# Performance work log

Measured on AMD Instinct MI355X. Metric: run time of the kernel, lower is better.

## Reference

```python
import jax, jax.numpy as jnp
import numpy as np

HEADS = 2
BN_EPS = 1e-5


def _axial_self_attn(x, Wq, Wkv, Wout, bout):
    # x: (b, s, t, c) -- attend along t (the axial sequence dim)
    b, s, t, c = x.shape
    dh = c // HEADS
    q = (x @ Wq).reshape(b, s, t, HEADS, dh)
    k, v = jnp.split(x @ Wkv, 2, axis=-1)  # matches torch .chunk(2, dim=-1)
    k = k.reshape(b, s, t, HEADS, dh)
    v = v.reshape(b, s, t, HEADS, dh)
    dots = jnp.einsum('bsind,bsjnd->bsnij', q, k) * (dh ** -0.5)
    attn = jax.nn.softmax(dots, axis=-1)
    out = jnp.einsum('bsnij,bsjnd->bsind', attn, v).reshape(b, s, t, c)
    return out @ Wout + bout


def setup_inputs() -> dict:
    key = jax.random.key(0)
    ks = jax.random.split(key, 8)
    B, C, H, W = 8, 128, 256, 256
    E = 2 * C
    sd = 0.05
    return {
        'x': jax.random.normal(ks[0], (B, C, H, W), jnp.float32),
        'Wq_h': jax.random.normal(ks[1], (C, C), jnp.float32) * sd,
        'Wkv_h': jax.random.normal(ks[2], (C, 2 * C), jnp.float32) * sd,
        'Wout_h': jax.random.normal(ks[3], (C, C), jnp.float32) * sd,
        'bout_h': jnp.zeros((C,), jnp.float32),
        'Wq_w': jax.random.normal(ks[4], (C, C), jnp.float32) * sd,
        'Wkv_w': jax.random.normal(ks[5], (C, 2 * C), jnp.float32) * sd,
        'Wout_w': jax.random.normal(ks[6], (C, C), jnp.float32) * sd,
        'bout_w': jnp.zeros((C,), jnp.float32),
        'conv_w': jax.random.normal(ks[7], (E, E), jnp.float32) * sd,  # (in, out); torch conv weight[o,i,0,0].T
        'gamma': jnp.ones((E,), jnp.float32),
        'beta': jnp.zeros((E,), jnp.float32),
    }


def reference(x, Wq_h, Wkv_h, Wout_h, bout_h, Wq_w, Wkv_w, Wout_w, bout_w, conv_w, gamma, beta):
    B, C, H, W = x.shape
    # MaxPool2d(2)
    xp = x.reshape(B, C, H // 2, 2, W // 2, 2).max(axis=(3, 5))  # (B,C,H2,W2)
    xc = jnp.transpose(xp, (0, 2, 3, 1))  # (B,H2,W2,C) channels-last
    # AxialAttention, sum_axial_out=True: height-axis attn + width-axis attn
    a_h = _axial_self_attn(jnp.transpose(xc, (0, 2, 1, 3)), Wq_h, Wkv_h, Wout_h, bout_h)
    a_h = jnp.transpose(a_h, (0, 2, 1, 3))
    a_w = _axial_self_attn(xc, Wq_w, Wkv_w, Wout_w, bout_w)
    a = jax.nn.relu(a_h + a_w)
    # cat((x_attn, x), dim=channel) then conv1x1 -> relu -> BatchNorm (batch stats)
    y = jnp.concatenate([a, xc], axis=-1) @ conv_w  # (B,H2,W2,2C)
    y = jax.nn.relu(y)
    mean = y.mean(axis=(0, 1, 2))
    var = y.var(axis=(0, 1, 2))
    y = (y - mean) * jax.lax.rsqrt(var + BN_EPS) * gamma + beta
    return jnp.transpose(y, (0, 3, 1, 2))  # back to NCHW
```

## Files before the change

### kernel.cpp

```cpp
#include <hip/hip_runtime.h>
#include <hip/hip_bf16.h>


typedef short v8s __attribute__((ext_vector_type(8)));
typedef short v4s __attribute__((ext_vector_type(4)));
typedef float v4f __attribute__((ext_vector_type(4)));
typedef float v4flt __attribute__((ext_vector_type(4)));

#define LSA 136
#define LSC 264
#define LSY 72
#define LSP 130

static __device__ __forceinline__ short f2bf(float f){
  __hip_bfloat16 h = __float2bfloat16(f);
  return __builtin_bit_cast(short, h);
}
static __device__ __forceinline__ float bf2f(short s){
  unsigned u = ((unsigned)(unsigned short)s) << 16;
  return __builtin_bit_cast(float, u);
}

__global__ void prep_kernel(const float* __restrict__ Wq_h, const float* __restrict__ Wkv_h,
                            const float* __restrict__ Wout_h, const float* __restrict__ Wq_w,
                            const float* __restrict__ Wkv_w, const float* __restrict__ Wout_w,
                            const float* __restrict__ conv_w, short* __restrict__ wt,
                            float* __restrict__ stats){
  int idx = blockIdx.x * 256 + threadIdx.x;
  if (idx < 8192) stats[idx] = 0.0f;
  const float* src; int K, O, base;
  if      (idx <  16384){ base = 0;      K=128; O=128; src=Wq_h;  }
  else if (idx <  49152){ base = 16384;  K=128; O=256; src=Wkv_h; }
  else if (idx <  65536){ base = 49152;  K=128; O=128; src=Wout_h;}
  else if (idx <  81920){ base = 65536;  K=128; O=128; src=Wq_w;  }
  else if (idx < 114688){ base = 81920;  K=128; O=256; src=Wkv_w; }
  else if (idx < 131072){ base = 114688; K=128; O=128; src=Wout_w;}
  else                  { base = 131072; K=256; O=256; src=conv_w;}
  int local = idx - base;
  int o = local / K, i = local - o * K;
  wt[idx] = f2bf(src[i * O + o]);
}

__global__ __launch_bounds__(256, 4)
void pool_kernel(const float* __restrict__ x, short* __restrict__ xp){
  __shared__ short t_[128*LSP];
  int bx = blockIdx.x;
  int b = bx >> 7, i = bx & 127;
  int tid = (int)threadIdx.x;
  int j2 = tid & 63;
  int cq = tid >> 6;
  for (int rep = 0; rep < 32; ++rep){
    int c = cq*32 + rep;
    const float* p0 = x + (((b*128 + c)*256 + 2*i)*256 + 4*j2);
    v4flt a  = *(const v4flt*)p0;
    v4flt bb = *(const v4flt*)(p0 + 256);
    t_[(2*j2)*LSP + c]   = f2bf(fmaxf(fmaxf(a[0], a[1]), fmaxf(bb[0], bb[1])));
    t_[(2*j2+1)*LSP + c] = f2bf(fmaxf(fmaxf(a[2], a[3]), fmaxf(bb[2], bb[3])));
  }
  __syncthreads();
  int obase = ((b*128 + i)*128)*128;
  for (int rep = 0; rep < 8; ++rep){
    int idx = rep*256 + tid;
    int row = idx >> 4, seg = idx & 15;
    *(v8s*)(xp + obase + row*128 + seg*8) = *(const v8s*)(&t_[row*LSP + seg*8]);
  }
}

__global__ __launch_bounds__(512, 6)
void attn_kernel(const short* __restrict__ xp, const short* __restrict__ wt,
                 const float* __restrict__ bout_h, const float* __restrict__ bout_w,
                 short* __restrict__ ah, short* __restrict__ aw){
  __shared__ short A[128*LSA];
  __shared__ short WB[64*LSA];

  const int bx = blockIdx.x;
  const int dir = bx & 1;
  const int sb = bx >> 1;
  const int b = sb >> 7, s = sb & 127;
  const int tid = (int)threadIdx.x;
  const int w = tid >> 6;
  const int lane = tid & 63;
  const int l15 = lane & 15, l4 = lane >> 4;

  const short* Wq   = wt + dir*65536;
  const short* Wk   = Wq + 16384;
  const short* Wv   = Wq + 32768;
  const short* Wout = Wq + 49152;
  const float* bsrc = dir ? bout_w : bout_h;
  short*       ao   = dir ? aw : ah;

  const int trow = 16*w + l15;
  const int xbase = dir ? (((b*128 + s)*128 + trow)*128)
                        : (((b*128 + trow)*128 + s)*128);
  v8s av[4];
  #pragma unroll
  for (int kk = 0; kk < 4; ++kk)
    av[kk] = *(const v8s*)(xp + xbase + kk*32 + l4*8);

  v8s rw0, rw1;
#define LOAD_H(SRC, HF)                                                  \
  { rw0 = *(const v8s*)((SRC) + (64*(HF) + (tid>>4))*128 + (tid&15)*8);  \
    rw1 = *(const v8s*)((SRC) + (64*(HF) + 32 + (tid>>4))*128 + (tid&15)*8); }
#define WRITE_H()                                                        \
  { *(v8s*)(&WB[(tid>>4)*LSA + (tid&15)*8]) = rw0;                       \
    *(v8s*)(&WB[(32 + (tid>>4))*LSA + (tid&15)*8]) = rw1; }

#define QK_HALF(HF)                                                      \
  { _Pragma("unroll")                                                    \
    for (int tcl = 0; tcl < 4; ++tcl){                                   \
      int tc = 4*(HF) + tcl;                                             \
      v4f d = {0.f,0.f,0.f,0.f};                                         \
      _Pragma("unroll")                                                  \
      for (int kk = 0; kk < 4; ++kk){                                    \
        v8s bf = *(const v8s*)(&WB[(tcl*16 + l15)*LSA + kk*32 + l4*8]);  \
        d = __builtin_amdgcn_mfma_f32_16x16x32_bf16(av[kk], bf, d, 0, 0, 0); \
      }                                                                  \
      _Pragma("unroll")                                                  \
      for (int r = 0; r < 4; ++r)                                        \
        A[(16*w + 4*l4 + r)*LSA + 16*tc + l15] = f2bf(d[r]);             \
    } }

#define V_HALF(HF)                                                       \
  { _Pragma("unroll")                                                    \
    for (int tcl = 0; tcl < 4; ++tcl){                                   \
      int tc = 4*(HF) + tcl;                                             \
      v4f d = {0.f,0.f,0.f,0.f};                                         \
      _Pragma("unroll")                                                  \
      for (int kk = 0; kk < 4; ++kk){                                    \
        v8s bf = *(const v8s*)(&WB[(tcl*16 + l15)*LSA + kk*32 + l4*8]);  \
        d = __builtin_amdgcn_mfma_f32_16x16x32_bf16(av[kk], bf, d, 0, 0, 0); \
      }                                                                  \
      v4s pkv;                                                           \
      _Pragma("unroll")                                                  \
      for (int r = 0; r < 4; ++r) pkv[r] = f2bf(d[r]);                   \
      *(v4s*)(&A[(16*tc + l15)*LSA + 16*w + 4*l4]) = pkv;                \
    } }

#define OUTPROJ_HALF(HF)                                                 \
  { _Pragma("unroll")                                                    \
    for (int tcl = 0; tcl < 4; ++tcl){                                   \
      int tc = 4*(HF) + tcl;                                             \
      v4f d = {0.f,0.f,0.f,0.f};                                         \
      _Pragma("unroll")                                                  \
      for (int kk = 0; kk < 4; ++kk){                                    \
        v8s awf = *(const v8s*)(&WB[(tcl*16 + l15)*LSA + kk*32 + l4*8]); \
        d = __builtin_amdgcn_mfma_f32_16x16x32_bf16(awf, ob[kk], d, 0, 0, 0); \
      }                                                                  \
      v4f bias = *(const v4f*)(bsrc + 16*tc + 4*l4);                     \
      v4s z;                                                             \
      _Pragma("unroll")                                                  \
      for (int r = 0; r < 4; ++r) z[r] = f2bf(d[r] + bias[r]);           \
      *(v4s*)(&A[(16*w + l15)*LSA + 16*tc + 4*l4]) = z;                  \
    } }

  LOAD_H(Wq, 0);
  WRITE_H(); __syncthreads();
  LOAD_H(Wq, 1);
  QK_HALF(0); __syncthreads();
  WRITE_H(); __syncthreads();
  LOAD_H(Wk, 0);
  QK_HALF(1);
  v8s bq[2][2];
  #pragma unroll
  for (int h = 0; h < 2; ++h)
    #pragma unroll
    for (int kk = 0; kk < 2; ++kk)
      bq[h][kk] = *(const v8s*)(&A[(16*w + l15)*LSA + h*64 + kk*32 + l4*8]);
  __syncthreads();

  WRITE_H(); __syncthreads();
  LOAD_H(Wk, 1);
  QK_HALF(0); __syncthreads();
  WRITE_H(); __syncthreads();
  LOAD_H(Wv, 0);
  QK_HALF(1); __syncthreads();
  WRITE_H();

  v4s pk[2][8];
  #pragma unroll
  for (int h = 0; h < 2; ++h){
    v4f st[8];
    #pragma unroll
    for (int jt = 0; jt < 8; ++jt){
      v4f d = {0.f,0.f,0.f,0.f};
      #pragma unroll
      for (int kk = 0; kk < 2; ++kk){
        v8s ak = *(const v8s*)(&A[(16*jt + l15)*LSA + h*64 + kk*32 + l4*8]);
        d = __builtin_amdgcn_mfma_f32_16x16x32_bf16(ak, bq[h][kk], d, 0, 0, 0);
      }
      st[jt] = d;
    }
    float mx = -1e30f;
    #pragma unroll
    for (int jt = 0; jt < 8; ++jt)
      #pragma unroll
      for (int r = 0; r < 4; ++r) mx = fmaxf(mx, st[jt][r]);
    mx = fmaxf(mx, __shfl_xor(mx, 16));
    mx = fmaxf(mx, __shfl_xor(mx, 32));
    float sm = 0.f;
    #pragma unroll
    for (int jt = 0; jt < 8; ++jt)
      #pragma unroll
      for (int r = 0; r < 4; ++r){
        float e = __expf((st[jt][r] - mx) * 0.125f);
        st[jt][r] = e; sm += e;
      }
    sm += __shfl_xor(sm, 16);
    sm += __shfl_xor(sm, 32);
    float inv = 1.0f / sm;
    #pragma unroll
    for (int jt = 0; jt < 8; ++jt)
      #pragma unroll
      for (int r = 0; r < 4; ++r) pk[h][jt][r] = f2bf(st[jt][r] * inv);
  }
  __syncthreads();

  v8s pa[2][4];
  #pragma unroll
  for (int h = 0; h < 2; ++h){
    #pragma unroll
    for (int jt = 0; jt < 8; ++jt)
      *(v4s*)(&A[(16*w + l15)*LSA + 16*jt + 4*l4]) = pk[h][jt];
    #pragma unroll
    for (int kk = 0; kk < 4; ++kk)
      pa[h][kk] = *(const v8s*)(&A[(16*w + l15)*LSA + kk*32 + l4*8]);
  }
  __syncthreads();

  LOAD_H(Wv, 1);
  V_HALF(0); __syncthreads();
  WRITE_H(); __syncthreads();
  LOAD_H(Wout, 0);
  V_HALF(1); __syncthreads();
  WRITE_H();

  v4f ot[2][4];
  #pragma unroll
  for (int h = 0; h < 2; ++h)
    #pragma unroll
    for (int tc = 0; tc < 4; ++tc){
      v4f d = {0.f,0.f,0.f,0.f};
      #pragma unroll
      for (int kk = 0; kk < 4; ++kk){
        v8s vf = *(const v8s*)(&A[(64*h + 16*tc + l15)*LSA + kk*32 + l4*8]);
        d = __builtin_amdgcn_mfma_f32_16x16x32_bf16(vf, pa[h][kk], d, 0, 0, 0);
      }
      ot[h][tc] = d;
    }
  __syncthreads();

  #pragma unroll
  for (int h = 0; h < 2; ++h)
    #pragma unroll
    for (int tc = 0; tc < 4; ++tc){
      v4s pko;
      #pragma unroll
      for (int r = 0; r < 4; ++r) pko[r] = f2bf(ot[h][tc][r]);
      *(v4s*)(&A[(16*w + l15)*LSA + 64*h + 16*tc + 4*l4]) = pko;
    }
  v8s ob[4];
  #pragma unroll
  for (int kk = 0; kk < 4; ++kk)
    ob[kk] = *(const v8s*)(&A[(16*w + l15)*LSA + kk*32 + l4*8]);
  LOAD_H(Wout, 1);
  OUTPROJ_HALF(0);
  __syncthreads();
  WRITE_H(); __syncthreads();
  OUTPROJ_HALF(1);
  __syncthreads();

  int obase = ((b*128 + s)*128)*128;
  #pragma unroll
  for (int r = 0; r < 4; ++r){
    int idx = (r*512 + tid) * 8;
    int t = idx >> 7, c = idx & 127;
    *(v8s*)(ao + obase + t*128 + c) = *(const v8s*)(&A[t*LSA + c]);
  }
#undef LOAD_H
#undef WRITE_H
#undef QK_HALF
#undef V_HALF
#undef OUTPROJ_HALF
}

__global__ __launch_bounds__(512, 4)
void conv_kernel(const short* __restrict__ ah, const short* __restrict__ aw,
                 const short* __restrict__ xp, const short* __restrict__ wt,
                 short* __restrict__ yb, float* __restrict__ stats){
  __shared__ short cats[256*LSY];
  __shared__ float lsum[256];
  __shared__ float lsq[256];
  const short* convT = wt + 131072;
  int bx = blockIdx.x;
  int half = bx & 1;
  int row = bx >> 1;
  int b = row >> 7, ii = row & 127;
  int tid = (int)threadIdx.x;
  int wv = tid >> 6, lane = tid & 63, l15 = lane & 15, l4 = lane >> 4;
  if (tid < 256){ lsum[tid] = 0.f; lsq[tid] = 0.f; }

  v8s wf[2][8];
  #pragma unroll
  for (int x = 0; x < 2; ++x)
    #pragma unroll
    for (int kk = 0; kk < 8; ++kk)
      wf[x][kk] = *(const v8s*)(convT + (((wv + 8*x)*16 + l15)*256) + kk*32 + l4*8);

  #pragma unroll
  for (int r = 0; r < 2; ++r){
    int idx = (r*512 + tid) * 8;
    int t = idx >> 7, c = idx & 127;
    int tg = 64*half + t;
    v8s hv = *(const v8s*)(ah + ((b*128 + tg)*128 + ii)*128 + c);
    v8s wv_ = *(const v8s*)(aw + ((b*128 + ii)*128 + tg)*128 + c);
    v8s o;
    #pragma unroll
    for (int k = 0; k < 8; ++k)
      o[k] = f2bf(fmaxf(bf2f(hv[k]) + bf2f(wv_[k]), 0.f));
    *(v8s*)(&cats[t*LSC + c]) = o;
    *(v8s*)(&cats[t*LSC + 128 + c]) =
        *(const v8s*)(xp + ((b*128 + ii)*128 + tg)*128 + c);
  }
  __syncthreads();

  v4s ypk[2][4];
  float s1[2] = {0.f,0.f}, s2[2] = {0.f,0.f};
  #pragma unroll
  for (int tt = 0; tt < 4; ++tt){
    v4f d0 = {0.f,0.f,0.f,0.f}, d1 = {0.f,0.f,0.f,0.f};
    #pragma unroll
    for (int kk = 0; kk < 8; ++kk){
      v8s af = *(const v8s*)(&cats[(16*tt + l15)*LSC + kk*32 + l4*8]);
      d0 = __builtin_amdgcn_mfma_f32_16x16x32_bf16(af, wf[0][kk], d0, 0, 0, 0);
      d1 = __builtin_amdgcn_mfma_f32_16x16x32_bf16(af, wf[1][kk], d1, 0, 0, 0);
    }
    #pragma unroll
    for (int r = 0; r < 4; ++r){
      float y0 = fmaxf(d0[r], 0.f), y1 = fmaxf(d1[r], 0.f);
      ypk[0][tt][r] = f2bf(y0); ypk[1][tt][r] = f2bf(y1);
      s1[0] += y0; s2[0] += y0*y0;
      s1[1] += y1; s2[1] += y1*y1;
    }
  }
  #pragma unroll
  for (int x = 0; x < 2; ++x){
    s1[x] += __shfl_xor(s1[x], 16); s1[x] += __shfl_xor(s1[x], 32);
    s2[x] += __shfl_xor(s2[x], 16); s2[x] += __shfl_xor(s2[x], 32);
  }
  if (l4 == 0){
    #pragma unroll
    for (int x = 0; x < 2; ++x){
      int e = (wv + 8*x)*16 + l15;
      atomicAdd(&lsum[e], s1[x]);
      atomicAdd(&lsq[e],  s2[x]);
    }
  }
  __syncthreads();
  #pragma unroll
  for (int x = 0; x < 2; ++x)
    #pragma unroll
    for (int tt = 0; tt < 4; ++tt)
      *(v4s*)(&cats[((wv + 8*x)*16 + l15)*LSY + 16*tt + 4*l4]) = ypk[x][tt];
  __syncthreads();
  #pragma unroll
  for (int r = 0; r < 4; ++r){
    int idxv = r*512 + tid;
    int e = idxv >> 3, jseg = idxv & 7;
    *(v8s*)(yb + ((b*256 + e)*128 + ii)*128 + 64*half + jseg*8) =
        *(const v8s*)(&cats[e*LSY + jseg*8]);
  }
  if (tid < 256){
    int c = bx & 15;
    atomicAdd(&stats[c*512 + tid],       lsum[tid]);
    atomicAdd(&stats[c*512 + 256 + tid], lsq[tid]);
  }
}

__global__ void bn_kernel(const short* __restrict__ yb, float* __restrict__ out,
                          const float* __restrict__ stats,
                          const float* __restrict__ gamma, const float* __restrict__ beta){
  const float invn = 1.0f / 131072.0f;
  int bx = blockIdx.x;
  int e = bx & 255;
  float s1 = 0.f, s2 = 0.f;
  #pragma unroll
  for (int c = 0; c < 16; ++c){
    s1 += stats[c*512 + e];
    s2 += stats[c*512 + 256 + e];
  }
  float m   = s1 * invn;
  float var = s2 * invn - m * m;
  float sc  = gamma[e] * rsqrtf(var + 1e-5f);
  float sh  = beta[e] - m * sc;
  int base = bx * 16384;
  int tid = (int)threadIdx.x;
  for (int rep = 0; rep < 8; ++rep){
    int idx = base + (rep*256 + tid)*8;
    v8s yv = *(const v8s*)(yb + idx);
    v4f o1, o2;
    #pragma unroll
    for (int r = 0; r < 4; ++r){
      o1[r] = bf2f(yv[r])   * sc + sh;
      o2[r] = bf2f(yv[4+r]) * sc + sh;
    }
    *(v4f*)(out + idx)     = o1;
    *(v4f*)(out + idx + 4) = o2;
  }
}

extern "C" void kernel_launch(void* const* d_in, const int* in_sizes, int n_in,
                              void* d_out, int out_size, void* d_ws, size_t ws_size,
                              hipStream_t stream){
  const float* x      = (const float*)d_in[0];
  const float* Wq_h   = (const float*)d_in[1];
  const float* Wkv_h  = (const float*)d_in[2];
  const float* Wout_h = (const float*)d_in[3];
  const float* bout_h = (const float*)d_in[4];
  const float* Wq_w   = (const float*)d_in[5];
  const float* Wkv_w  = (const float*)d_in[6];
  const float* Wout_w = (const float*)d_in[7];
  const float* bout_w = (const float*)d_in[8];
  const float* conv_w = (const float*)d_in[9];
  const float* gamma  = (const float*)d_in[10];
  const float* beta   = (const float*)d_in[11];
  float* out = (float*)d_out;

  char* ws = (char*)d_ws;
  short* xp    = (short*)(ws);
  short* ah    = (short*)(ws +  33554432);
  short* aw    = (short*)(ws +  67108864);
  short* yb    = (short*)(ws + 100663296);
  short* wt    = (short*)(ws + 167772160);
  float* stats = (float*)(ws + 168165376);

  prep_kernel<<<768, 256, 0, stream>>>(Wq_h, Wkv_h, Wout_h, Wq_w, Wkv_w, Wout_w,
                                       conv_w, wt, stats);
  pool_kernel<<<1024, 256, 0, stream>>>(x, xp);
  attn_kernel<<<2048, 512, 0, stream>>>(xp, wt, bout_h, bout_w, ah, aw);
  conv_kernel<<<2048, 512, 0, stream>>>(ah, aw, xp, wt, yb, stats);
  bn_kernel<<<2048, 256, 0, stream>>>(yb, out, stats, gamma, beta);
}
```

Baseline: 257.7 us.

## Double-buffer weight quarters in attention and split pooling across channel halves

The attention kernel now stages weights in 32-row quarters through two LDS buffers. The next quarter's global load and LDS write are interleaved with MFMA work on the current buffer, so fewer syncthreads stall on weight staging. The pooling kernel is split into two blocks per row, each covering half the channels, with a smaller LDS tile and higher occupancy bounds. The attention schedule adds more barriers per phase and is intricate, so a mistake in buffer reuse ordering could cause races.

```diff
diff --git a/kernel.cpp b/kernel.cpp
--- a/kernel.cpp
+++ b/kernel.cpp
@@ -10,7 +10,7 @@
 #define LSA 136
 #define LSC 264
 #define LSY 72
-#define LSP 130
+#define LSQ 66
 
 static __device__ __forceinline__ short f2bf(float f){
   __hip_bfloat16 h = __float2bfloat16(f);
@@ -41,28 +41,32 @@
   wt[idx] = f2bf(src[i * O + o]);
 }
 
-__global__ __launch_bounds__(256, 4)
+__global__ __launch_bounds__(256, 8)
 void pool_kernel(const float* __restrict__ x, short* __restrict__ xp){
-  __shared__ short t_[128*LSP];
+  __shared__ short t_[128*LSQ];
   int bx = blockIdx.x;
-  int b = bx >> 7, i = bx & 127;
+  int chalf = bx & 1;
+  int row = bx >> 1;
+  int b = row >> 7, i = row & 127;
   int tid = (int)threadIdx.x;
   int j2 = tid & 63;
   int cq = tid >> 6;
-  for (int rep = 0; rep < 32; ++rep){
-    int c = cq*32 + rep;
+  for (int rep = 0; rep < 16; ++rep){
+    int cl = cq*16 + rep;
+    int c = chalf*64 + cl;
     const float* p0 = x + (((b*128 + c)*256 + 2*i)*256 + 4*j2);
     v4flt a  = *(const v4flt*)p0;
     v4flt bb = *(const v4flt*)(p0 + 256);
-    t_[(2*j2)*LSP + c]   = f2bf(fmaxf(fmaxf(a[0], a[1]), fmaxf(bb[0], bb[1])));
-    t_[(2*j2+1)*LSP + c] = f2bf(fmaxf(fmaxf(a[2], a[3]), fmaxf(bb[2], bb[3])));
-  }
-  __syncthreads();
-  int obase = ((b*128 + i)*128)*128;
-  for (int rep = 0; rep < 8; ++rep){
+    t_[(2*j2)*LSQ + cl]   = f2bf(fmaxf(fmaxf(a[0], a[1]), fmaxf(bb[0], bb[1])));
+    t_[(2*j2+1)*LSQ + cl] = f2bf(fmaxf(fmaxf(a[2], a[3]), fmaxf(bb[2], bb[3])));
+  }
+  __syncthreads();
+  int obase = ((b*128 + i)*128)*128 + chalf*64;
+  #pragma unroll
+  for (int rep = 0; rep < 4; ++rep){
     int idx = rep*256 + tid;
-    int row = idx >> 4, seg = idx & 15;
-    *(v8s*)(xp + obase + row*128 + seg*8) = *(const v8s*)(&t_[row*LSP + seg*8]);
+    int r_ = idx >> 3, seg = idx & 7;
+    *(v8s*)(xp + obase + r_*128 + seg*8) = *(const v8s*)(&t_[r_*LSQ + seg*8]);
   }
 }
 
@@ -71,7 +75,7 @@
                  const float* __restrict__ bout_h, const float* __restrict__ bout_w,
                  short* __restrict__ ah, short* __restrict__ aw){
   __shared__ short A[128*LSA];
-  __shared__ short WB[64*LSA];
+  __shared__ short WB[2][32*LSA];
 
   const int bx = blockIdx.x;
   const int dir = bx & 1;
@@ -81,6 +85,8 @@
   const int w = tid >> 6;
   const int lane = tid & 63;
   const int l15 = lane & 15, l4 = lane >> 4;
+  const int qrow = tid >> 4;
+  const int qseg = tid & 15;
 
   const short* Wq   = wt + dir*65536;
   const short* Wk   = Wq + 16384;
@@ -97,22 +103,18 @@
   for (int kk = 0; kk < 4; ++kk)
     av[kk] = *(const v8s*)(xp + xbase + kk*32 + l4*8);
 
-  v8s rw0, rw1;
-#define LOAD_H(SRC, HF)                                                  \
-  { rw0 = *(const v8s*)((SRC) + (64*(HF) + (tid>>4))*128 + (tid&15)*8);  \
-    rw1 = *(const v8s*)((SRC) + (64*(HF) + 32 + (tid>>4))*128 + (tid&15)*8); }
-#define WRITE_H()                                                        \
-  { *(v8s*)(&WB[(tid>>4)*LSA + (tid&15)*8]) = rw0;                       \
-    *(v8s*)(&WB[(32 + (tid>>4))*LSA + (tid&15)*8]) = rw1; }
-
-#define QK_HALF(HF)                                                      \
+  v8s rw;
+#define LOAD_Q(SRC, QI)  rw = *(const v8s*)((SRC) + (32*(QI) + qrow)*128 + qseg*8);
+#define WRITE_Q(SL)      *(v8s*)(&WB[SL][qrow*LSA + qseg*8]) = rw;
+
+#define QK_Q(SL, TB)                                                     \
   { _Pragma("unroll")                                                    \
-    for (int tcl = 0; tcl < 4; ++tcl){                                   \
-      int tc = 4*(HF) + tcl;                                             \
+    for (int tcl = 0; tcl < 2; ++tcl){                                   \
+      int tc = (TB) + tcl;                                               \
       v4f d = {0.f,0.f,0.f,0.f};                                         \
       _Pragma("unroll")                                                  \
       for (int kk = 0; kk < 4; ++kk){                                    \
-        v8s bf = *(const v8s*)(&WB[(tcl*16 + l15)*LSA + kk*32 + l4*8]);  \
+        v8s bf = *(const v8s*)(&WB[SL][(tcl*16 + l15)*LSA + kk*32 + l4*8]); \
         d = __builtin_amdgcn_mfma_f32_16x16x32_bf16(av[kk], bf, d, 0, 0, 0); \
       }                                                                  \
       _Pragma("unroll")                                                  \
@@ -120,14 +122,14 @@
         A[(16*w + 4*l4 + r)*LSA + 16*tc + l15] = f2bf(d[r]);             \
     } }
 
-#define V_HALF(HF)                                                       \
+#define V_Q(SL, TB)                                                      \
   { _Pragma("unroll")                                                    \
-    for (int tcl = 0; tcl < 4; ++tcl){                                   \
-      int tc = 4*(HF) + tcl;                                             \
+    for (int tcl = 0; tcl < 2; ++tcl){                                   \
+      int tc = (TB) + tcl;                                               \
       v4f d = {0.f,0.f,0.f,0.f};                                         \
       _Pragma("unroll")                                                  \
       for (int kk = 0; kk < 4; ++kk){                                    \
-        v8s bf = *(const v8s*)(&WB[(tcl*16 + l15)*LSA + kk*32 + l4*8]);  \
+        v8s bf = *(const v8s*)(&WB[SL][(tcl*16 + l15)*LSA + kk*32 + l4*8]); \
         d = __builtin_amdgcn_mfma_f32_16x16x32_bf16(av[kk], bf, d, 0, 0, 0); \
       }                                                                  \
       v4s pkv;                                                           \
@@ -136,14 +138,14 @@
       *(v4s*)(&A[(16*tc + l15)*LSA + 16*w + 4*l4]) = pkv;                \
     } }
 
-#define OUTPROJ_HALF(HF)                                                 \
+#define OP_Q(SL, TB)                                                     \
   { _Pragma("unroll")                                                    \
-    for (int tcl = 0; tcl < 4; ++tcl){                                   \
-      int tc = 4*(HF) + tcl;                                             \
+    for (int tcl = 0; tcl < 2; ++tcl){                                   \
+      int tc = (TB) + tcl;                                               \
       v4f d = {0.f,0.f,0.f,0.f};                                         \
       _Pragma("unroll")                                                  \
       for (int kk = 0; kk < 4; ++kk){                                    \
-        v8s awf = *(const v8s*)(&WB[(tcl*16 + l15)*LSA + kk*32 + l4*8]); \
+        v8s awf = *(const v8s*)(&WB[SL][(tcl*16 + l15)*LSA + kk*32 + l4*8]); \
         d = __builtin_amdgcn_mfma_f32_16x16x32_bf16(awf, ob[kk], d, 0, 0, 0); \
       }                                                                  \
       v4f bias = *(const v4f*)(bsrc + 16*tc + 4*l4);                     \
@@ -153,13 +155,16 @@
       *(v4s*)(&A[(16*w + l15)*LSA + 16*tc + 4*l4]) = z;                  \
     } }
 
-  LOAD_H(Wq, 0);
-  WRITE_H(); __syncthreads();
-  LOAD_H(Wq, 1);
-  QK_HALF(0); __syncthreads();
-  WRITE_H(); __syncthreads();
-  LOAD_H(Wk, 0);
-  QK_HALF(1);
+  LOAD_Q(Wq,0); WRITE_Q(0);
+  LOAD_Q(Wq,1);
+  __syncthreads();
+  QK_Q(0,0); WRITE_Q(1); LOAD_Q(Wq,2);
+  __syncthreads();
+  QK_Q(1,2); WRITE_Q(0); LOAD_Q(Wq,3);
+  __syncthreads();
+  QK_Q(0,4); WRITE_Q(1); LOAD_Q(Wk,0);
+  __syncthreads();
+  QK_Q(1,6); WRITE_Q(0); LOAD_Q(Wk,1);
   v8s bq[2][2];
   #pragma unroll
   for (int h = 0; h < 2; ++h)
@@ -168,14 +173,16 @@
       bq[h][kk] = *(const v8s*)(&A[(16*w + l15)*LSA + h*64 + kk*32 + l4*8]);
   __syncthreads();
 
-  WRITE_H(); __syncthreads();
-  LOAD_H(Wk, 1);
-  QK_HALF(0); __syncthreads();
-  WRITE_H(); __syncthreads();
-  LOAD_H(Wv, 0);
-  QK_HALF(1); __syncthreads();
-  WRITE_H();
-
+  QK_Q(0,0); WRITE_Q(1); LOAD_Q(Wk,2);
+  __syncthreads();
+  QK_Q(1,2); WRITE_Q(0); LOAD_Q(Wk,3);
+  __syncthreads();
+  QK_Q(0,4); WRITE_Q(1); LOAD_Q(Wv,0);
+  __syncthreads();
+  QK_Q(1,6); WRITE_Q(0); LOAD_Q(Wv,1);
+  __syncthreads();
+
+  WRITE_Q(1);
   v4s pk[2][8];
   #pragma unroll
   for (int h = 0; h < 2; ++h){
@@ -213,6 +220,7 @@
       #pragma unroll
       for (int r = 0; r < 4; ++r) pk[h][jt][r] = f2bf(st[jt][r] * inv);
   }
+  LOAD_Q(Wv,2);
   __syncthreads();
 
   v8s pa[2][4];
@@ -227,13 +235,16 @@
   }
   __syncthreads();
 
-  LOAD_H(Wv, 1);
-  V_HALF(0); __syncthreads();
-  WRITE_H(); __syncthreads();
-  LOAD_H(Wout, 0);
-  V_HALF(1); __syncthreads();
-  WRITE_H();
-
+  V_Q(0,0);
+  __syncthreads();
+  V_Q(1,2); WRITE_Q(0); LOAD_Q(Wv,3);
+  __syncthreads();
+  V_Q(0,4); WRITE_Q(1);
+  __syncthreads();
+  V_Q(1,6); LOAD_Q(Wout,0);
+  __syncthreads();
+
+  WRITE_Q(0);
   v4f ot[2][4];
   #pragma unroll
   for (int h = 0; h < 2; ++h)
@@ -247,6 +258,7 @@
       }
       ot[h][tc] = d;
     }
+  LOAD_Q(Wout,1);
   __syncthreads();
 
   #pragma unroll
@@ -262,11 +274,13 @@
   #pragma unroll
   for (int kk = 0; kk < 4; ++kk)
     ob[kk] = *(const v8s*)(&A[(16*w + l15)*LSA + kk*32 + l4*8]);
-  LOAD_H(Wout, 1);
-  OUTPROJ_HALF(0);
-  __syncthreads();
-  WRITE_H(); __syncthreads();
-  OUTPROJ_HALF(1);
+  OP_Q(0,0); WRITE_Q(1); LOAD_Q(Wout,2);
+  __syncthreads();
+  OP_Q(1,2); WRITE_Q(0); LOAD_Q(Wout,3);
+  __syncthreads();
+  OP_Q(0,4); WRITE_Q(1);
+  __syncthreads();
+  OP_Q(1,6);
   __syncthreads();
 
   int obase = ((b*128 + s)*128)*128;
@@ -276,11 +290,11 @@
     int t = idx >> 7, c = idx & 127;
     *(v8s*)(ao + obase + t*128 + c) = *(const v8s*)(&A[t*LSA + c]);
   }
-#undef LOAD_H
-#undef WRITE_H
-#undef QK_HALF
-#undef V_HALF
-#undef OUTPROJ_HALF
+#undef LOAD_Q
+#undef WRITE_Q
+#undef QK_Q
+#undef V_Q
+#undef OP_Q
 }
 
 __global__ __launch_bounds__(512, 4)
@@ -435,7 +449,7 @@
 
   prep_kernel<<<768, 256, 0, stream>>>(Wq_h, Wkv_h, Wout_h, Wq_w, Wkv_w, Wout_w,
                                        conv_w, wt, stats);
-  pool_kernel<<<1024, 256, 0, stream>>>(x, xp);
+  pool_kernel<<<2048, 256, 0, stream>>>(x, xp);
   attn_kernel<<<2048, 512, 0, stream>>>(xp, wt, bout_h, bout_w, ah, aw);
   conv_kernel<<<2048, 512, 0, stream>>>(ah, aw, xp, wt, yb, stats);
   bn_kernel<<<2048, 256, 0, stream>>>(yb, out, stats, gamma, beta);
```

Result: no change. 253.7 us (median of 2 runs) (-1.5%).
